# Kernel optimization log

Hardware: AMD Instinct MI355X
Metric: run time of the kernel (lower is better)

The kernel has to match this reference:

```python
import jax, jax.numpy as jnp
import numpy as np

B, C, H, W = 8, 128, 64, 64


def setup_inputs() -> dict:
    key = jax.random.key(0)
    ks = jax.random.split(key, 4)
    s = 1.0 / np.sqrt(C)
    return {
        "x": jax.random.normal(ks[0], (B, C, H, W), dtype=jnp.float32),
        "Wq": jax.random.normal(ks[1], (C, C), dtype=jnp.float32) * s,
        "bq": jnp.zeros((C,), dtype=jnp.float32),
        "Wk": jax.random.normal(ks[2], (C, C), dtype=jnp.float32) * s,
        "bk": jnp.zeros((C,), dtype=jnp.float32),
        "Wv": jax.random.normal(ks[3], (C, C), dtype=jnp.float32) * s,
        "bv": jnp.zeros((C,), dtype=jnp.float32),
    }


def reference(x, Wq, bq, Wk, bk, Wv, bv):
    b, c, h, w = x.shape
    xf = x.reshape(b, c, h * w)  # [B, C, N]
    # 1x1 convs are per-pixel CxC matmuls (weight[out,in] contracted over in)
    q = jnp.einsum("oc,bcn->bon", Wq, xf) + bq[None, :, None]
    k = jnp.einsum("oc,bcn->bon", Wk, xf) + bk[None, :, None]
    v = jnp.einsum("oc,bcn->bon", Wv, xf) + bv[None, :, None]
    scale = 1.0 / jnp.sqrt(jnp.asarray(c, dtype=x.dtype))
    attn = jnp.einsum("bcn,bcm->bnm", q, k) * scale  # [B, N, N]
    attn = jax.nn.softmax(attn, axis=-1)
    out = jnp.einsum("bnm,bcm->bcn", attn, v)  # [B, C, N]
    return out.reshape(b, c, h, w) + x
```

## Files before the change

kernel.cpp:

```cpp
#include <hip/hip_runtime.h>

#define B_ 8
#define C_ 128
#define N_ 4096
#define SCALE 0.08838834764831845f

typedef __attribute__((ext_vector_type(8))) short short8;
typedef __attribute__((ext_vector_type(4))) short short4v;
typedef __attribute__((ext_vector_type(4))) float f32x4;

__device__ inline unsigned short f2b(float f) {
    unsigned int u;
    asm("v_cvt_pk_bf16_f32 %0, %1, %2" : "=v"(u) : "v"(f), "v"(f));
    return (unsigned short)u;
}

__device__ inline void gld_lds16(const void* g, void* l) {
    __builtin_amdgcn_global_load_lds(
        (const __attribute__((address_space(1))) unsigned int*)g,
        (__attribute__((address_space(3))) unsigned int*)l, 16, 0, 0);
}

__global__ __launch_bounds__(256) void qkv_mfma(
    const float* __restrict__ x,
    const float* __restrict__ Wq, const float* __restrict__ bq,
    const float* __restrict__ Wk, const float* __restrict__ bk,
    const float* __restrict__ Wv, const float* __restrict__ bv,
    float* __restrict__ q, unsigned short* __restrict__ kTs,
    unsigned short* __restrict__ vS)
{
    __shared__ __align__(16) short Xs[64 * 128];
    __shared__ __align__(16) float Obuf[64 * 132];

    const int t    = threadIdx.x;
    const int w    = t >> 6;
    const int lane = t & 63;
    const int l15  = lane & 15;
    const int quad = lane >> 4;

    const int b  = blockIdx.x & 7;
    const int n0 = (blockIdx.x >> 3) * 64;
    const long base = (long)b * C_ * N_;

    auto load_af = [&](const float* __restrict__ W, short8 (&af)[2][4]) {
        #pragma unroll
        for (int ot = 0; ot < 2; ++ot) {
            const int o = 32 * w + 16 * ot + l15;
            #pragma unroll
            for (int ks = 0; ks < 4; ++ks) {
                const float4 a0 = *(const float4*)(const void*)(W + o * C_ + ks * 32 + quad * 8);
                const float4 a1 = *(const float4*)(const void*)(W + o * C_ + ks * 32 + quad * 8 + 4);
                union { unsigned int u[4]; short8 s; } pk;
                asm("v_cvt_pk_bf16_f32 %0, %1, %2" : "=v"(pk.u[0]) : "v"(a0.x), "v"(a0.y));
                asm("v_cvt_pk_bf16_f32 %0, %1, %2" : "=v"(pk.u[1]) : "v"(a0.z), "v"(a0.w));
                asm("v_cvt_pk_bf16_f32 %0, %1, %2" : "=v"(pk.u[2]) : "v"(a1.x), "v"(a1.y));
                asm("v_cvt_pk_bf16_f32 %0, %1, %2" : "=v"(pk.u[3]) : "v"(a1.z), "v"(a1.w));
                af[ot][ks] = pk.s;
            }
        }
    };

    auto mfma_pass = [&](const short8 (&af)[2][4], f32x4 (&acc)[2][4]) {
        #pragma unroll
        for (int ot = 0; ot < 2; ++ot)
            #pragma unroll
            for (int nt = 0; nt < 4; ++nt)
                acc[ot][nt] = (f32x4){0.f, 0.f, 0.f, 0.f};
        #pragma unroll
        for (int nt = 0; nt < 4; ++nt) {
            const int n = nt * 16 + l15;
            short8 bx[4];
            #pragma unroll
            for (int ks = 0; ks < 4; ++ks)
                bx[ks] = *(const short8*)(const void*)(Xs + n * 128 + (((ks * 4 + quad) ^ l15) << 3));
            #pragma unroll
            for (int ot = 0; ot < 2; ++ot)
                #pragma unroll
                for (int ks = 0; ks < 4; ++ks)
                    acc[ot][nt] = __builtin_amdgcn_mfma_f32_16x16x32_bf16(af[ot][ks], bx[ks], acc[ot][nt], 0, 0, 0);
        }
    };

    short8 afA[2][4], afB[2][4];
    load_af(Wq, afA);

    #pragma unroll
    for (int it = 0; it < 8; ++it) {
        const int c  = (t >> 4) + it * 16;
        const int n4 = (t & 15) * 4;
        const float4 xv = *(const float4*)(const void*)(x + base + (long)c * N_ + n0 + n4);
        const int bc = c >> 3, cl = c & 7;
        Xs[(n4 + 0) * 128 + ((bc ^ ((n4 + 0) & 15)) << 3) + cl] = (short)f2b(xv.x);
        Xs[(n4 + 1) * 128 + ((bc ^ ((n4 + 1) & 15)) << 3) + cl] = (short)f2b(xv.y);
        Xs[(n4 + 2) * 128 + ((bc ^ ((n4 + 2) & 15)) << 3) + cl] = (short)f2b(xv.z);
        Xs[(n4 + 3) * 128 + ((bc ^ ((n4 + 3) & 15)) << 3) + cl] = (short)f2b(xv.w);
    }
    __syncthreads();

    {
        load_af(Wv, afB);
        f32x4 acc[2][4];
        mfma_pass(afA, acc);
        #pragma unroll
        for (int ot = 0; ot < 2; ++ot)
            #pragma unroll
            for (int r = 0; r < 4; ++r) {
                const int o = 32 * w + 16 * ot + quad * 4 + r;
                const float bb = bq[o];
                #pragma unroll
                for (int nt = 0; nt < 4; ++nt)
                    q[base + (long)o * N_ + n0 + nt * 16 + l15] = (acc[ot][nt][r] + bb) * SCALE;
            }
    }

    {
        load_af(Wk, afA);
        f32x4 acc[2][4];
        mfma_pass(afB, acc);
        #pragma unroll
        for (int ot = 0; ot < 2; ++ot)
            #pragma unroll
            for (int r = 0; r < 4; ++r) {
                const int o = 32 * w + 16 * ot + quad * 4 + r;
                const float bb = bv[o];
                #pragma unroll
                for (int nt = 0; nt < 4; ++nt)
                    Obuf[o * 66 + nt * 16 + l15] = acc[ot][nt][r] + bb;
            }
        __syncthreads();
        {
            const int o = t >> 1, half = (t & 1) * 32;
            const int sw = (o >> 1) & 3;
            #pragma unroll
            for (int bs = 0; bs < 4; ++bs) {
                const float4 v0 = *(const float4*)(const void*)(Obuf + o * 66 + half + bs * 8);
                const float4 v1 = *(const float4*)(const void*)(Obuf + o * 66 + half + bs * 8 + 4);
                union { unsigned int u[4]; short8 s; } pk;
                asm("v_cvt_pk_bf16_f32 %0, %1, %2" : "=v"(pk.u[0]) : "v"(v0.x), "v"(v0.y));
                asm("v_cvt_pk_bf16_f32 %0, %1, %2" : "=v"(pk.u[1]) : "v"(v0.z), "v"(v0.w));
                asm("v_cvt_pk_bf16_f32 %0, %1, %2" : "=v"(pk.u[2]) : "v"(v1.x), "v"(v1.y));
                asm("v_cvt_pk_bf16_f32 %0, %1, %2" : "=v"(pk.u[3]) : "v"(v1.z), "v"(v1.w));
                *(short8*)(void*)(vS + base + (long)o * N_ + n0 + half + ((bs ^ sw) << 3)) = pk.s;
            }
        }
        __syncthreads();
    }

    {
        f32x4 acc[2][4];
        mfma_pass(afA, acc);
        #pragma unroll
        for (int ot = 0; ot < 2; ++ot)
            #pragma unroll
            for (int r = 0; r < 4; ++r) {
                const int o = 32 * w + 16 * ot + quad * 4 + r;
                const float bb = bk[o];
                #pragma unroll
                for (int nt = 0; nt < 4; ++nt) {
                    const int n = nt * 16 + l15;
                    Obuf[n * 132 + (((o >> 3) ^ l15) << 3) + (o & 7)] = acc[ot][nt][r] + bb;
                }
            }
        __syncthreads();
        const int n = t >> 2, oh = (t & 3) * 32;
        #pragma unroll
        for (int i = 0; i < 32; i += 8) {
            const float4 k0 = *(const float4*)(const void*)(Obuf + n * 132 + oh + i);
            const float4 k1 = *(const float4*)(const void*)(Obuf + n * 132 + oh + i + 4);
            union { unsigned int u[4]; short8 s; } pk;
            asm("v_cvt_pk_bf16_f32 %0, %1, %2" : "=v"(pk.u[0]) : "v"(k0.x), "v"(k0.y));
            asm("v_cvt_pk_bf16_f32 %0, %1, %2" : "=v"(pk.u[1]) : "v"(k0.z), "v"(k0.w));
            asm("v_cvt_pk_bf16_f32 %0, %1, %2" : "=v"(pk.u[2]) : "v"(k1.x), "v"(k1.y));
            asm("v_cvt_pk_bf16_f32 %0, %1, %2" : "=v"(pk.u[3]) : "v"(k1.z), "v"(k1.w));
            *(short8*)(void*)(kTs + base + (long)(n0 + n) * C_ + oh + i) = pk.s;
        }
    }
}

__global__ __launch_bounds__(512, 4) void attn_mfma(
    const float* qg,
    const unsigned short* __restrict__ kTs,
    const unsigned short* __restrict__ vS,
    const float* __restrict__ xg,
    float* out)
{
    __shared__ union {
        struct {
            short V[2][2][4096];
            short Pb[2][2][2][32 * 40];
        } s;
        float Ot[64 * 130];
    } sm;
    __shared__ float Ls[2][2][32];
    __shared__ float linvA[64];

    const int t    = threadIdx.x;
    const int w    = t >> 6;
    const int g    = w >> 2;
    const int wq   = (w >> 1) & 1;
    const int h    = w & 1;
    const int sub  = w & 3;
    const int lane = t & 63;
    const int l15  = lane & 15;
    const int quad = lane >> 4;

    const int b  = blockIdx.x & 7;
    const int n0 = (blockIdx.x >> 3) * 64;
    const long base = (long)b * C_ * N_;

    const int query0 = n0 + 32 * wq;
    short8 qf[2][4];
    #pragma unroll
    for (int qh = 0; qh < 2; ++qh)
        #pragma unroll
        for (int ks = 0; ks < 4; ++ks) {
            short8 f;
            #pragma unroll
            for (int j = 0; j < 8; ++j) {
                const int c = ks * 32 + quad * 8 + j;
                f[j] = (short)f2b(qg[base + (long)c * N_ + query0 + qh * 16 + l15]);
            }
            qf[qh][ks] = f;
        }

    f32x4 acc[2][4];
    #pragma unroll
    for (int qh = 0; qh < 2; ++qh)
        #pragma unroll
        for (int ct = 0; ct < 4; ++ct) acc[qh][ct] = (f32x4){0.f, 0.f, 0.f, 0.f};
    f32x4 accS[2];
    accS[0] = (f32x4){0.f, 0.f, 0.f, 0.f};
    accS[1] = (f32x4){0.f, 0.f, 0.f, 0.f};
    short8 ones;
    #pragma unroll
    for (int j = 0; j < 8; ++j) ones[j] = (short)0x3F80;

    auto stageV = [&](int buf, int pair) {
        const int mt = pair * 2 + g;
        char* lV = (char*)sm.s.V[buf][g];
        #pragma unroll
        for (int jj = 0; jj < 2; ++jj) {
            const int d  = sub * 2048 + jj * 1024;
            const int dv = d + lane * 16;
            const int c  = dv >> 6;
            gld_lds16((const char*)(vS + base + (long)c * N_ + mt * 32) + (dv & 63), lV + d);
        }
    };

    const unsigned short* kp = kTs + base + (long)((g * 32 + h * 16 + l15) * C_);
    int ko[4];
    #pragma unroll
    for (int ks = 0; ks < 4; ++ks) ko[ks] = (((ks * 4 + quad) ^ l15) << 3);
    short8 kf[4];

    stageV(0, 0);
    #pragma unroll
    for (int ks = 0; ks < 4; ++ks) kf[ks] = *(const short8*)(const void*)(kp + ko[ks]);
    kp += 64 * C_;

    for (int i = 0; i < 64; ++i) {
        f32x4 sc[2];
        sc[0] = (f32x4){0.f, 0.f, 0.f, 0.f};
        sc[1] = (f32x4){0.f, 0.f, 0.f, 0.f};
        __builtin_amdgcn_s_setprio(1);
        #pragma unroll
        for (int qh = 0; qh < 2; ++qh)
            #pragma unroll
            for (int ks = 0; ks < 4; ++ks)
                sc[qh] = __builtin_amdgcn_mfma_f32_16x16x32_bf16(qf[qh][ks], kf[ks], sc[qh], 0, 0, 0);
        __builtin_amdgcn_s_setprio(0);

        if (i < 63) {
            #pragma unroll
            for (int ks = 0; ks < 4; ++ks) kf[ks] = *(const short8*)(const void*)(kp + ko[ks]);
            kp += 64 * C_;
        }

        short* Pw = sm.s.Pb[i & 1][g][wq];
        #pragma unroll
        for (int qh = 0; qh < 2; ++qh)
            #pragma unroll
            for (int r = 0; r < 4; ++r)
                Pw[(qh * 16 + quad * 4 + r) * 40 + h * 16 + l15] = (short)f2b(__expf(sc[qh][r]));

        if (i < 63) asm volatile("s_waitcnt vmcnt(4)" ::: "memory");
        else        asm volatile("s_waitcnt vmcnt(0)" ::: "memory");
        asm volatile("s_waitcnt lgkmcnt(0)" ::: "memory");
        __builtin_amdgcn_s_barrier();
        __builtin_amdgcn_sched_barrier(0);

        if (i < 63) stageV((i + 1) & 1, i + 1);

        const short* Vb = sm.s.V[i & 1][g];
        const short8 pf0 = *(const short8*)(const void*)(Pw + (l15) * 40 + quad * 8);
        const short8 pf1 = *(const short8*)(const void*)(Pw + (16 + l15) * 40 + quad * 8);
        __builtin_amdgcn_s_setprio(1);
        if (h == 0) {
            accS[0] = __builtin_amdgcn_mfma_f32_16x16x32_bf16(pf0, ones, accS[0], 0, 0, 0);
            accS[1] = __builtin_amdgcn_mfma_f32_16x16x32_bf16(pf1, ones, accS[1], 0, 0, 0);
        }
        #pragma unroll
        for (int ct = 0; ct < 4; ++ct) {
            const int ch = h * 64 + ct * 16 + l15;
            const short8 vf = *(const short8*)(const void*)(Vb + ch * 32 + ((quad ^ ((l15 >> 1) & 3)) << 3));
            acc[0][ct] = __builtin_amdgcn_mfma_f32_16x16x32_bf16(pf0, vf, acc[0][ct], 0, 0, 0);
            acc[1][ct] = __builtin_amdgcn_mfma_f32_16x16x32_bf16(pf1, vf, acc[1][ct], 0, 0, 0);
        }
        __builtin_amdgcn_s_setprio(0);
    }

    if (h == 0 && l15 == 0) {
        #pragma unroll
        for (int qh = 0; qh < 2; ++qh)
            #pragma unroll
            for (int r = 0; r < 4; ++r)
                Ls[g][wq][qh * 16 + quad * 4 + r] = accS[qh][r];
    }
    __syncthreads();
    if (g == 0) {
        #pragma unroll
        for (int qh = 0; qh < 2; ++qh)
            #pragma unroll
            for (int ct = 0; ct < 4; ++ct)
                #pragma unroll
                for (int r = 0; r < 4; ++r)
                    sm.Ot[(32 * wq + qh * 16 + quad * 4 + r) * 130 + h * 64 + ct * 16 + l15] = acc[qh][ct][r];
    }
    __syncthreads();
    if (g == 1) {
        #pragma unroll
        for (int qh = 0; qh < 2; ++qh)
            #pragma unroll
            for (int ct = 0; ct < 4; ++ct)
                #pragma unroll
                for (int r = 0; r < 4; ++r)
                    sm.Ot[(32 * wq + qh * 16 + quad * 4 + r) * 130 + h * 64 + ct * 16 + l15] += acc[qh][ct][r];
    } else if (h == 0 && l15 == 0) {
        #pragma unroll
        for (int qh = 0; qh < 2; ++qh)
            #pragma unroll
            for (int r = 0; r < 4; ++r) {
                const int r32 = qh * 16 + quad * 4 + r;
                linvA[32 * wq + r32] = 1.0f / fmaxf(Ls[0][wq][r32] + Ls[1][wq][r32], 1e-20f);
            }
    }
    __syncthreads();

    const int c  = t >> 2;
    const int nh = (t & 3) * 16;
    const long gb = base + (long)c * N_ + n0 + nh;
    #pragma unroll
    for (int i = 0; i < 16; i += 4) {
        const float4 xs = *(const float4*)(const void*)(xg + gb + i);
        float4 rv;
        rv.x = sm.Ot[(nh + i + 0) * 130 + c] * linvA[nh + i + 0] + xs.x;
        rv.y = sm.Ot[(nh + i + 1) * 130 + c] * linvA[nh + i + 1] + xs.y;
        rv.z = sm.Ot[(nh + i + 2) * 130 + c] * linvA[nh + i + 2] + xs.z;
        rv.w = sm.Ot[(nh + i + 3) * 130 + c] * linvA[nh + i + 3] + xs.w;
        *(float4*)(void*)(out + gb + i) = rv;
    }
}

extern "C" void kernel_launch(void* const* d_in, const int* in_sizes, int n_in,
                              void* d_out, int out_size, void* d_ws, size_t ws_size,
                              hipStream_t stream) {
    const float* x  = (const float*)d_in[0];
    const float* Wq = (const float*)d_in[1];
    const float* bq = (const float*)d_in[2];
    const float* Wk = (const float*)d_in[3];
    const float* bk = (const float*)d_in[4];
    const float* Wv = (const float*)d_in[5];
    const float* bv = (const float*)d_in[6];
    float* out = (float*)d_out;

    const long BCN = (long)B_ * C_ * N_;
    unsigned short* kTs = (unsigned short*)d_ws;
    unsigned short* vS  = kTs + BCN;

    qkv_mfma<<<512, 256, 0, stream>>>(x, Wq, bq, Wk, bk, Wv, bv, out, kTs, vS);
    attn_mfma<<<B_ * (N_ / 64), 512, 0, stream>>>(out, kTs, vS, x, out);
}
```

Baseline: 190.5 us.

## Fuse Q projection into attention kernel and write V directly without LDS staging

Moves the Q 1x1-conv projection out of the first kernel and into the attention kernel's prologue. Each attention block projects its 64 queries from x in LDS with MFMA and reads Q fragments from a swizzled LDS buffer. This removes the fp32 Q round-trip through global memory and the strided per-element Q loads. The first kernel also writes bf16 V straight from registers with scalar 2-byte stores instead of staging through LDS for packed 16-byte stores. That trades extra per-block Wq loads and MFMA work in the attention kernel, plus less coalesced V stores, for fewer global bytes.

```diff
diff --git a/kernel.cpp b/kernel.cpp
--- a/kernel.cpp
+++ b/kernel.cpp
@@ -21,13 +21,11 @@
         (__attribute__((address_space(3))) unsigned int*)l, 16, 0, 0);
 }
 
-__global__ __launch_bounds__(256) void qkv_mfma(
+__global__ __launch_bounds__(256) void kv_mfma(
     const float* __restrict__ x,
-    const float* __restrict__ Wq, const float* __restrict__ bq,
     const float* __restrict__ Wk, const float* __restrict__ bk,
     const float* __restrict__ Wv, const float* __restrict__ bv,
-    float* __restrict__ q, unsigned short* __restrict__ kTs,
-    unsigned short* __restrict__ vS)
+    unsigned short* __restrict__ kTs, unsigned short* __restrict__ vS)
 {
     __shared__ __align__(16) short Xs[64 * 128];
     __shared__ __align__(16) float Obuf[64 * 132];
@@ -82,7 +80,7 @@
     };
 
     short8 afA[2][4], afB[2][4];
-    load_af(Wq, afA);
+    load_af(Wv, afA);
 
     #pragma unroll
     for (int it = 0; it < 8; ++it) {
@@ -98,57 +96,28 @@
     __syncthreads();
 
     {
-        load_af(Wv, afB);
+        load_af(Wk, afB);
         f32x4 acc[2][4];
         mfma_pass(afA, acc);
-        #pragma unroll
-        for (int ot = 0; ot < 2; ++ot)
-            #pragma unroll
-            for (int r = 0; r < 4; ++r) {
-                const int o = 32 * w + 16 * ot + quad * 4 + r;
-                const float bb = bq[o];
-                #pragma unroll
-                for (int nt = 0; nt < 4; ++nt)
-                    q[base + (long)o * N_ + n0 + nt * 16 + l15] = (acc[ot][nt][r] + bb) * SCALE;
-            }
-    }
-
-    {
-        load_af(Wk, afA);
-        f32x4 acc[2][4];
-        mfma_pass(afB, acc);
         #pragma unroll
         for (int ot = 0; ot < 2; ++ot)
             #pragma unroll
             for (int r = 0; r < 4; ++r) {
                 const int o = 32 * w + 16 * ot + quad * 4 + r;
                 const float bb = bv[o];
+                const int sw = ((o >> 1) & 3) << 3;
                 #pragma unroll
-                for (int nt = 0; nt < 4; ++nt)
-                    Obuf[o * 66 + nt * 16 + l15] = acc[ot][nt][r] + bb;
-            }
-        __syncthreads();
-        {
-            const int o = t >> 1, half = (t & 1) * 32;
-            const int sw = (o >> 1) & 3;
-            #pragma unroll
-            for (int bs = 0; bs < 4; ++bs) {
-                const float4 v0 = *(const float4*)(const void*)(Obuf + o * 66 + half + bs * 8);
-                const float4 v1 = *(const float4*)(const void*)(Obuf + o * 66 + half + bs * 8 + 4);
-                union { unsigned int u[4]; short8 s; } pk;
-                asm("v_cvt_pk_bf16_f32 %0, %1, %2" : "=v"(pk.u[0]) : "v"(v0.x), "v"(v0.y));
-                asm("v_cvt_pk_bf16_f32 %0, %1, %2" : "=v"(pk.u[1]) : "v"(v0.z), "v"(v0.w));
-                asm("v_cvt_pk_bf16_f32 %0, %1, %2" : "=v"(pk.u[2]) : "v"(v1.x), "v"(v1.y));
-                asm("v_cvt_pk_bf16_f32 %0, %1, %2" : "=v"(pk.u[3]) : "v"(v1.z), "v"(v1.w));
-                *(short8*)(void*)(vS + base + (long)o * N_ + n0 + half + ((bs ^ sw) << 3)) = pk.s;
-            }
-        }
-        __syncthreads();
+                for (int nt = 0; nt < 4; ++nt) {
+                    const int n = nt * 16 + l15;
+                    const int ns = (n & 32) | ((((n >> 3) & 3) << 3) ^ sw) | (n & 7);
+                    vS[base + (long)o * N_ + n0 + ns] = f2b(acc[ot][nt][r] + bb);
+                }
+            }
     }
 
     {
         f32x4 acc[2][4];
-        mfma_pass(afA, acc);
+        mfma_pass(afB, acc);
         #pragma unroll
         for (int ot = 0; ot < 2; ++ot)
             #pragma unroll
@@ -178,7 +147,7 @@
 }
 
 __global__ __launch_bounds__(512, 4) void attn_mfma(
-    const float* qg,
+    const float* __restrict__ Wq, const float* __restrict__ bq,
     const unsigned short* __restrict__ kTs,
     const unsigned short* __restrict__ vS,
     const float* __restrict__ xg,
@@ -189,6 +158,10 @@
             short V[2][2][4096];
             short Pb[2][2][2][32 * 40];
         } s;
+        struct {
+            short Xst[64 * 128];
+            short Qs[64 * 128];
+        } pre;
         float Ot[64 * 130];
     } sm;
     __shared__ float Ls[2][2][32];
@@ -208,19 +181,68 @@
     const int n0 = (blockIdx.x >> 3) * 64;
     const long base = (long)b * C_ * N_;
 
-    const int query0 = n0 + 32 * wq;
+    #pragma unroll
+    for (int it = 0; it < 4; ++it) {
+        const int c  = (t >> 4) + it * 32;
+        const int n4 = (t & 15) * 4;
+        const float4 xv = *(const float4*)(const void*)(xg + base + (long)c * N_ + n0 + n4);
+        const int bc = c >> 3, cl = c & 7;
+        sm.pre.Xst[(n4 + 0) * 128 + ((bc ^ ((n4 + 0) & 15)) << 3) + cl] = (short)f2b(xv.x);
+        sm.pre.Xst[(n4 + 1) * 128 + ((bc ^ ((n4 + 1) & 15)) << 3) + cl] = (short)f2b(xv.y);
+        sm.pre.Xst[(n4 + 2) * 128 + ((bc ^ ((n4 + 2) & 15)) << 3) + cl] = (short)f2b(xv.z);
+        sm.pre.Xst[(n4 + 3) * 128 + ((bc ^ ((n4 + 3) & 15)) << 3) + cl] = (short)f2b(xv.w);
+    }
+    __syncthreads();
+    {
+        short8 aq[4];
+        const int o = 16 * w + l15;
+        #pragma unroll
+        for (int ks = 0; ks < 4; ++ks) {
+            const float4 a0 = *(const float4*)(const void*)(Wq + o * C_ + ks * 32 + quad * 8);
+            const float4 a1 = *(const float4*)(const void*)(Wq + o * C_ + ks * 32 + quad * 8 + 4);
+            union { unsigned int u[4]; short8 s; } pk;
+            asm("v_cvt_pk_bf16_f32 %0, %1, %2" : "=v"(pk.u[0]) : "v"(a0.x), "v"(a0.y));
+            asm("v_cvt_pk_bf16_f32 %0, %1, %2" : "=v"(pk.u[1]) : "v"(a0.z), "v"(a0.w));
+            asm("v_cvt_pk_bf16_f32 %0, %1, %2" : "=v"(pk.u[2]) : "v"(a1.x), "v"(a1.y));
+            asm("v_cvt_pk_bf16_f32 %0, %1, %2" : "=v"(pk.u[3]) : "v"(a1.z), "v"(a1.w));
+            aq[ks] = pk.s;
+        }
+        f32x4 qa[4];
+        #pragma unroll
+        for (int nt = 0; nt < 4; ++nt) qa[nt] = (f32x4){0.f, 0.f, 0.f, 0.f};
+        #pragma unroll
+        for (int nt = 0; nt < 4; ++nt) {
+            const int n = nt * 16 + l15;
+            #pragma unroll
+            for (int ks = 0; ks < 4; ++ks) {
+                const short8 bx = *(const short8*)(const void*)(
+                    sm.pre.Xst + n * 128 + (((ks * 4 + quad) ^ l15) << 3));
+                qa[nt] = __builtin_amdgcn_mfma_f32_16x16x32_bf16(aq[ks], bx, qa[nt], 0, 0, 0);
+            }
+        }
+        const float4 bb = *(const float4*)(const void*)(bq + 16 * w + quad * 4);
+        #pragma unroll
+        for (int r = 0; r < 4; ++r) {
+            const int oo = 16 * w + quad * 4 + r;
+            const float br = r == 0 ? bb.x : r == 1 ? bb.y : r == 2 ? bb.z : bb.w;
+            #pragma unroll
+            for (int nt = 0; nt < 4; ++nt) {
+                const int n = nt * 16 + l15;
+                sm.pre.Qs[n * 128 + (((oo >> 3) ^ (n & 15)) << 3) + (oo & 7)] =
+                    (short)f2b((qa[nt][r] + br) * SCALE);
+            }
+        }
+    }
+    __syncthreads();
+
     short8 qf[2][4];
     #pragma unroll
     for (int qh = 0; qh < 2; ++qh)
         #pragma unroll
         for (int ks = 0; ks < 4; ++ks) {
-            short8 f;
-            #pragma unroll
-            for (int j = 0; j < 8; ++j) {
-                const int c = ks * 32 + quad * 8 + j;
-                f[j] = (short)f2b(qg[base + (long)c * N_ + query0 + qh * 16 + l15]);
-            }
-            qf[qh][ks] = f;
+            const int query = 32 * wq + qh * 16 + l15;
+            qf[qh][ks] = *(const short8*)(const void*)(
+                sm.pre.Qs + query * 128 + (((ks * 4 + quad) ^ l15) << 3));
         }
 
     f32x4 acc[2][4];
@@ -377,6 +399,6 @@
     unsigned short* kTs = (unsigned short*)d_ws;
     unsigned short* vS  = kTs + BCN;
 
-    qkv_mfma<<<512, 256, 0, stream>>>(x, Wq, bq, Wk, bk, Wv, bv, out, kTs, vS);
-    attn_mfma<<<B_ * (N_ / 64), 512, 0, stream>>>(out, kTs, vS, x, out);
+    kv_mfma<<<512, 256, 0, stream>>>(x, Wk, bk, Wv, bv, kTs, vS);
+    attn_mfma<<<B_ * (N_ / 64), 512, 0, stream>>>(Wq, bq, kTs, vS, x, out);
 }
```

Measured after the change: 181.4 us (median of 2 runs). -4.8%, faster.
